# Kernel optimization log

Hardware: AMD Instinct MI355X
Metric: run time of the kernel (lower is better)

The kernel has to match this reference:

```python
import jax, jax.numpy as jnp
import numpy as np

# Rs_hidden = [(16,0),(16,1)] -> 16 scalar irreps (dim 1) then 16 vector irreps (dim 3)
B, N, M = 4, 80, 16
CH = M + 3 * M  # 64 channels
RADII = jnp.linspace(0.0, 1.0, 3)
GAMMA = 1.0 / (0.5 ** 2)  # gaussian rbf width = radii spacing
EPS = 1e-6

_lc = np.zeros((3, 3, 3), np.float32)
for i, j, k in [(0, 1, 2), (1, 2, 0), (2, 0, 1)]:
    _lc[i, j, k] = 1.0
    _lc[i, k, j] = -1.0
LC = jnp.asarray(_lc)  # Levi-Civita


def _si(t, w0, w1):
    """SelfInteraction: per-l mixing of multiplicities. t: [B, mi0 + 3*mi1, ...]."""
    mi0, mi1 = w0.shape[1], w1.shape[1]
    s = t[:, :mi0]
    v = t[:, mi0:].reshape(t.shape[0], mi1, 3, *t.shape[2:])
    os = jnp.einsum('om,nm...->no...', w0, s)
    ov = jnp.einsum('om,nmi...->noi...', w1, v)
    ov = ov.reshape(ov.shape[0], ov.shape[1] * 3, *ov.shape[3:])
    return jnp.concatenate([os, ov], axis=1)


def _norm_act(t, act):
    """NormActivation: scalar irreps -> act(x); vector irreps -> x * act(||x||)/||x||. Channel axis 1."""
    s = act(t[:, :M])
    v = t[:, M:].reshape(t.shape[0], M, 3, *t.shape[2:])
    n = jnp.sqrt(jnp.sum(v * v, axis=2, keepdims=True) + EPS)
    v = (v * act(n) / n).reshape(t.shape[0], 3 * M, *t.shape[2:])
    return jnp.concatenate([s, v], axis=1)


def _gate_mul(gate, target):
    """gate_normwise_multiply: multiply each irrep block of target by the L2 norm of the
    corresponding gate block (norm over the irrep components, channel axis 1)."""
    gs = jnp.abs(gate[:, :M])
    gv = gate[:, M:].reshape(gate.shape[0], M, 3, *gate.shape[2:])
    gn = jnp.sqrt(jnp.sum(gv * gv, axis=2) + EPS)
    factor = jnp.concatenate([gs, jnp.repeat(gn, 3, axis=1)], axis=1)
    return factor * target


def _interleave(a_t, b_t):
    """Interleave per-(m,l) blocks: [a_l0, b_l0, a_l1, b_l1] -> Rs_hidden_double layout."""
    return jnp.concatenate([a_t[:, :M], b_t[:, :M], a_t[:, M:], b_t[:, M:]], axis=1)


def _kernel(h_nei_diff, w_k00, w_k10, w_k01, w_k11):
    """SE3 point kernel for l in {0,1}, J<=2. Returns K[n,b,a,d,c] with d,c in irrep layout."""
    rad = jnp.sqrt(jnp.sum(h_nei_diff ** 2, axis=-1) + EPS)      # [B,N,N]
    nh = h_nei_diff / rad[..., None]                              # unit vectors
    rbf = jnp.exp(-GAMMA * (rad[..., None] - RADII) ** 2)        # [B,N,N,3]
    K00 = jnp.einsum('uvk,...k->...uv', w_k00, rbf)              # [B,N,N,M,M]
    K10 = jnp.einsum('uvk,...k,...i->...uiv', w_k10, rbf, nh).reshape(B, N, N, 3 * M, M)
    K01 = jnp.einsum('uvk,...k,...j->...uvj', w_k01, rbf, nh).reshape(B, N, N, M, 3 * M)
    RJ = jnp.einsum('juvk,...k->j...uv', w_k11, rbf)             # [3,B,N,N,M,M]
    eye = jnp.eye(3, dtype=rbf.dtype)
    cross = jnp.einsum('ijk,...k->...ij', LC, nh)                # J=1 basis
    outer = nh[..., :, None] * nh[..., None, :] - eye / 3.0      # J=2 basis
    base = (RJ[0][..., None, None] * eye
            + RJ[1][..., None, None] * cross[..., None, None, :, :]
            + RJ[2][..., None, None] * outer[..., None, None, :, :])  # [B,N,N,u,v,i,j]
    K11 = jnp.transpose(base, (0, 1, 2, 3, 5, 4, 6)).reshape(B, N, N, 3 * M, 3 * M)
    top = jnp.concatenate([K00, K01], axis=-1)
    bot = jnp.concatenate([K10, K11], axis=-1)
    return jnp.concatenate([top, bot], axis=-2)                  # [B,N,N,CH,CH]


def setup_inputs() -> dict:
    key = jax.random.key(0)
    ks = jax.random.split(key, 16)
    sc = 0.1
    d = {
        'x': jax.random.normal(ks[0], (B, CH, N), jnp.float32),
        'h_nei': jax.random.normal(ks[1], (B, CH, N), jnp.float32),
        'h_nei_diff': jax.random.normal(ks[2], (B, N, N, 3), jnp.float32),
        'mask': jax.random.uniform(ks[3], (B, N, N), jnp.float32),
        'w_k00': jax.random.normal(ks[4], (M, M, 3), jnp.float32) * sc,
        'w_k10': jax.random.normal(ks[5], (M, M, 3), jnp.float32) * sc,
        'w_k01': jax.random.normal(ks[6], (M, M, 3), jnp.float32) * sc,
        'w_k11': jax.random.normal(ks[7], (3, M, M, 3), jnp.float32) * sc,
        'si_z_w0': jax.random.normal(ks[8], (M, 2 * M), jnp.float32) * sc,
        'si_z_w1': jax.random.normal(ks[9], (M, 2 * M), jnp.float32) * sc,
        'si_r1_w0': jax.random.normal(ks[10], (M, M), jnp.float32) * sc,
        'si_r1_w1': jax.random.normal(ks[11], (M, M), jnp.float32) * sc,
        'si_r2_w0': jax.random.normal(ks[12], (M, M), jnp.float32) * sc,
        'si_r2_w1': jax.random.normal(ks[13], (M, M), jnp.float32) * sc,
        'si_ph_w0': jax.random.normal(ks[14], (M, 2 * M), jnp.float32) * sc,
        'si_ph_w1': jax.random.normal(ks[15], (M, 2 * M), jnp.float32) * sc,
    }
    return d


def reference(x, h_nei, h_nei_diff, mask, w_k00, w_k10, w_k01, w_k11,
              si_z_w0, si_z_w1, si_r1_w0, si_r1_w1, si_r2_w0, si_r2_w1,
              si_ph_w0, si_ph_w1):
    Kmat = _kernel(h_nei_diff, w_k00, w_k10, w_k01, w_k11)
    # masked neighbor conv: h_conv[n,d,b,a] = sum_c h_nei[n,c,a] K[n,b,a,d,c] mask[n,b,a]
    h_conv = jnp.einsum('nca,nbadc,nba->ndba', h_nei, Kmat, mask)
    sum_h = h_conv.sum(axis=-1)                                   # [B,CH,N]
    z = _norm_act(_si(_interleave(x, sum_h), si_z_w0, si_z_w1), jax.nn.sigmoid)
    r1 = _si(x, si_r1_w0, si_r1_w1)                               # [B,CH,N]
    r2 = _si(h_conv.reshape(B, CH, N * N), si_r2_w0, si_r2_w1).reshape(B, CH, N, N)
    r = _norm_act(r1[:, :, None, :] + r2, jax.nn.sigmoid)         # [B,CH,N,N]
    gated = _gate_mul(r, h_conv)
    sum_g = gated.sum(axis=-1)                                    # [B,CH,N]
    pre_h = _norm_act(_si(_interleave(x, sum_g), si_ph_w0, si_ph_w1), jnp.tanh)
    new_h = sum_h + _gate_mul(z, pre_h + sum_h)
    return new_h
```

## Files before the change

### kernel.cpp

```cpp
#include <hip/hip_runtime.h>
#include <math.h>

#define Bq 4
#define Nq 80
#define CHq 64
#define GAMMAq 4.0f
#define EPSq 1e-6f
#define PCWL 100
#define NQUAD 24


__global__ __launch_bounds__(192) void se3_precomp(
    const float* __restrict__ h_nei,
    const float* __restrict__ x,
    const float* __restrict__ w00,
    const float* __restrict__ w10,
    const float* __restrict__ w01,
    const float* __restrict__ w11,
    const float* __restrict__ wr10,
    const float* __restrict__ wr11,
    const float* __restrict__ wr20,
    const float* __restrict__ wr21,
    float* __restrict__ pc)
{
    const int L   = blockIdx.x & 7;
    const int idx = blockIdx.x >> 3;
    const int n   = L >> 1;
    const int a   = (L & 1) * 40 + idx;
    const int na  = n * Nq + a;
    const int tid = threadIdx.x;

    __shared__ float hsh[64];
    __shared__ float xsh[64];
    __shared__ float w00s[784], w10s[784], w01s[784];
    __shared__ float w11s[3][784];
    __shared__ float wr10s[272], wr11s[272];
    __shared__ float psh[2][42][16];
    __shared__ float r1sh[2][4][16];
    __shared__ float pout[16][PCWL];

    if (tid < 64)       hsh[tid]      = h_nei[(size_t)n * CHq * Nq + tid * Nq + a];
    else if (tid < 128) xsh[tid - 64] = x    [(size_t)n * CHq * Nq + (tid - 64) * Nq + a];

    for (int e = tid; e < 768; e += 192) {
        const int u = e / 48, r = e - u * 48;
        const int d = u * 49 + r;
        w00s[d]    = w00[e];
        w10s[d]    = w10[e];
        w01s[d]    = w01[e];
        w11s[0][d] = w11[e];
        w11s[1][d] = w11[768 + e];
        w11s[2][d] = w11[1536 + e];
    }
    for (int e = tid; e < 256; e += 192) {
        const int u = e >> 4, v = e & 15;
        wr10s[u * 17 + v] = wr10[e];
        wr11s[u * 17 + v] = wr11[e];
    }
    __syncthreads();

    if (tid < 128) {
        const int u    = tid & 15;
        const int q    = tid >> 4;
        const int half = q & 1;
        const int kk   = q >> 1;
        const int v0   = half * 8;

        if (kk < 3) {
            const int k = kk;
            float a00 = 0.f, a10 = 0.f;
            float c[3] = {0.f,0.f,0.f}, p0[3] = {0.f,0.f,0.f};
            float p1[3] = {0.f,0.f,0.f}, p2[3] = {0.f,0.f,0.f};
#pragma unroll
            for (int i = 0; i < 8; ++i) {
                const int v  = v0 + i;
                const int wi = u * 49 + v * 3 + k;
                const float s = hsh[v];
                a00 += w00s[wi] * s;
                a10 += w10s[wi] * s;
                const float w01v = w01s[wi];
                const float w110 = w11s[0][wi];
                const float w111 = w11s[1][wi];
                const float w112 = w11s[2][wi];
#pragma unroll
                for (int j = 0; j < 3; ++j) {
                    const float Vj = hsh[16 + v * 3 + j];
                    c[j]  += w01v * Vj;
                    p0[j] += w110 * Vj;
                    p1[j] += w111 * Vj;
                    p2[j] += w112 * Vj;
                }
            }
            psh[half][0 + k][u] = a00;
            psh[half][3 + k][u] = a10;
#pragma unroll
            for (int j = 0; j < 3; ++j) {
                psh[half][6  + k * 3 + j][u] = c[j];
                psh[half][15 + k * 3 + j][u] = p0[j];
                psh[half][24 + k * 3 + j][u] = p1[j];
                psh[half][33 + k * 3 + j][u] = p2[j];
            }
        } else {
            float r1s = 0.f, r1v[3] = {0.f, 0.f, 0.f};
#pragma unroll
            for (int i = 0; i < 8; ++i) {
                const int v = v0 + i;
                r1s += wr10s[u * 17 + v] * xsh[v];
                const float wv = wr11s[u * 17 + v];
#pragma unroll
                for (int j = 0; j < 3; ++j) r1v[j] += wv * xsh[16 + v * 3 + j];
            }
            r1sh[half][0][u] = r1s;
#pragma unroll
            for (int j = 0; j < 3; ++j) r1sh[half][1 + j][u] = r1v[j];
        }
    }
    __syncthreads();

    if (tid < 96) {
        const int u  = tid & 15;
        const int kk = tid >> 4;
#pragma unroll
        for (int c = kk * 7; c < kk * 7 + 7; ++c)
            pout[u][c] = psh[0][c][u] + psh[1][c][u];
        if (kk == 0) {
#pragma unroll
            for (int j = 0; j < 4; ++j)
                pout[u][42 + j] = r1sh[0][j][u] + r1sh[1][j][u];
            pout[u][46] = 0.f; pout[u][47] = 0.f;
#pragma unroll
            for (int j = 90; j < 96; ++j) pout[u][j] = 0.f;
        }
    }
    __syncthreads();

    if (tid < 96) {
        const int u  = tid & 15;
        const int kk = tid >> 4;
#pragma unroll
        for (int c = kk * 7; c < kk * 7 + 7; ++c) {
            const bool scalarType = (c < 3) || (c >= 6 && c < 15);
            const float* W = scalarType ? wr20 : wr21;
            float acc = 0.f;
#pragma unroll
            for (int v = 0; v < 16; ++v) acc += W[u * 16 + v] * pout[v][c];
            pout[u][48 + c] = acc;
        }
    }
    __syncthreads();

    {
        float4* dst = reinterpret_cast<float4*>(pc) + (size_t)na * (NQUAD * 16);
#pragma unroll
        for (int i = 0; i < 2; ++i) {
            const int qi = tid + i * 192;
            const int c4 = qi >> 4;
            const int u  = qi & 15;
            dst[c4 * 16 + u] = make_float4(pout[u][c4 * 4 + 0], pout[u][c4 * 4 + 1],
                                           pout[u][c4 * 4 + 2], pout[u][c4 * 4 + 3]);
        }
    }
}

__global__ __launch_bounds__(256, 1) void se3_main(
    const float* __restrict__ x,
    const float* __restrict__ hdiff,
    const float* __restrict__ mask,
    const float* __restrict__ wz0,
    const float* __restrict__ wz1,
    const float* __restrict__ wp0,
    const float* __restrict__ wp1,
    const float* __restrict__ pc,
    float* __restrict__ out)
{
    const int L     = blockIdx.x & 7;
    const int idx   = blockIdx.x >> 3;
    const int n     = L >> 1;
    const int bnode = (L & 1) * 40 + idx;
    const int tid   = threadIdx.x;
    const int g     = tid >> 4;
    const int u     = tid & 15;

    __shared__ float wsh[4][512];
    __shared__ float redW[4][8][16];
    __shared__ float sumHs[64], sumGs[64];

#pragma unroll
    for (int i = 0; i < 2; ++i) {
        const int widx = tid + i * 256;
        wsh[0][widx] = wz0[widx];
        wsh[1][widx] = wz1[widx];
        wsh[2][widx] = wp0[widx];
        wsh[3][widx] = wp1[widx];
    }

    const float* drow = hdiff + (size_t)(n * Nq + bnode) * Nq * 3;
    const float* mrow = mask  + (size_t)(n * Nq + bnode) * Nq;
    const float third = 1.0f / 3.0f;

    float dg[5][3], mg[5];
#pragma unroll
    for (int it = 0; it < 5; ++it) {
        const int a = it * 16 + g;
        dg[it][0] = drow[a * 3 + 0];
        dg[it][1] = drow[a * 3 + 1];
        dg[it][2] = drow[a * 3 + 2];
        mg[it]    = mrow[a];
    }

    const float4* pcbase = reinterpret_cast<const float4*>(pc)
                         + (size_t)(n * Nq) * (NQUAD * 16) + u;

    float shs = 0.f, shv0 = 0.f, shv1 = 0.f, shv2 = 0.f;
    float sgs = 0.f, sgv0 = 0.f, sgv1 = 0.f, sgv2 = 0.f;

    float pa[2][48], pb[2][44];

    {
        const float4* p4 = pcbase + (size_t)g * (NQUAD * 16);
#pragma unroll
        for (int i = 0; i < 12; ++i)
            *reinterpret_cast<float4*>(&pa[0][i * 4]) = p4[i * 16];
#pragma unroll
        for (int i = 0; i < 11; ++i)
            *reinterpret_cast<float4*>(&pb[0][i * 4]) = p4[(12 + i) * 16];
    }

#pragma unroll
    for (int it = 0; it < 5; ++it) {
        const int cur = it & 1, nxt = cur ^ 1;

        if (it < 4) {
            const int a2 = (it + 1) * 16 + g;
            const float4* p4 = pcbase + (size_t)a2 * (NQUAD * 16);
#pragma unroll
            for (int i = 0; i < 12; ++i)
                *reinterpret_cast<float4*>(&pa[nxt][i * 4]) = p4[i * 16];
#pragma unroll
            for (int i = 0; i < 11; ++i)
                *reinterpret_cast<float4*>(&pb[nxt][i * 4]) = p4[(12 + i) * 16];
        }

        const float d0 = dg[it][0], d1 = dg[it][1], d2 = dg[it][2];
        const float m  = mg[it];

        const float rad = sqrtf(d0 * d0 + d1 * d1 + d2 * d2 + EPSq);
        const float inv = 1.0f / rad;
        const float nh0 = d0 * inv, nh1 = d1 * inv, nh2 = d2 * inv;
        float rb[3];
        rb[0] = __expf(-GAMMAq * rad * rad);
        { float t1 = rad - 0.5f; rb[1] = __expf(-GAMMAq * t1 * t1); }
        { float t2 = rad - 1.0f; rb[2] = __expf(-GAMMAq * t2 * t2); }

        float as_ = 0.f, a10 = 0.f;
        float c01[3] = {0.f,0.f,0.f}, p0[3] = {0.f,0.f,0.f};
        float p1[3] = {0.f,0.f,0.f}, p2[3] = {0.f,0.f,0.f};
        float bs_ = 0.f, b10 = 0.f;
        float bc01[3] = {0.f,0.f,0.f}, bp0[3] = {0.f,0.f,0.f};
        float bp1[3] = {0.f,0.f,0.f}, bp2[3] = {0.f,0.f,0.f};
#pragma unroll
        for (int k = 0; k < 3; ++k) {
            const float r = rb[k];
            as_ += r * pa[cur][0 + k];
            a10 += r * pa[cur][3 + k];
            bs_ += r * pb[cur][0 + k];
            b10 += r * pb[cur][3 + k];
#pragma unroll
            for (int j = 0; j < 3; ++j) {
                c01[j]  += r * pa[cur][6  + k * 3 + j];
                p0[j]   += r * pa[cur][15 + k * 3 + j];
                p1[j]   += r * pa[cur][24 + k * 3 + j];
                p2[j]   += r * pa[cur][33 + k * 3 + j];
                bc01[j] += r * pb[cur][6  + k * 3 + j];
                bp0[j]  += r * pb[cur][15 + k * 3 + j];
                bp1[j]  += r * pb[cur][24 + k * 3 + j];
                bp2[j]  += r * pb[cur][33 + k * 3 + j];
            }
        }

        const float hcs = m * (as_ + c01[0] * nh0 + c01[1] * nh1 + c01[2] * nh2);
        const float cr0 = p1[1] * nh2 - p1[2] * nh1;
        const float cr1 = p1[2] * nh0 - p1[0] * nh2;
        const float cr2 = p1[0] * nh1 - p1[1] * nh0;
        const float pd  = p2[0] * nh0 + p2[1] * nh1 + p2[2] * nh2;
        const float hv0 = m * (nh0 * a10 + p0[0] + cr0 + nh0 * pd - p2[0] * third);
        const float hv1 = m * (nh1 * a10 + p0[1] + cr1 + nh1 * pd - p2[1] * third);
        const float hv2 = m * (nh2 * a10 + p0[2] + cr2 + nh2 * pd - p2[2] * third);

        const float r2s = m * (bs_ + bc01[0] * nh0 + bc01[1] * nh1 + bc01[2] * nh2);
        const float br0 = bp1[1] * nh2 - bp1[2] * nh1;
        const float br1 = bp1[2] * nh0 - bp1[0] * nh2;
        const float br2 = bp1[0] * nh1 - bp1[1] * nh0;
        const float bpd = bp2[0] * nh0 + bp2[1] * nh1 + bp2[2] * nh2;
        const float r2v0 = m * (nh0 * b10 + bp0[0] + br0 + nh0 * bpd - bp2[0] * third);
        const float r2v1 = m * (nh1 * b10 + bp0[1] + br1 + nh1 * bpd - bp2[1] * third);
        const float r2v2 = m * (nh2 * b10 + bp0[2] + br2 + nh2 * bpd - bp2[2] * third);

        const float r1s  = pa[cur][42];
        const float r1v0 = pa[cur][43], r1v1 = pa[cur][44], r1v2 = pa[cur][45];

        const float rs  = 1.0f / (1.0f + __expf(-(r1s + r2s)));
        const float wv0 = r1v0 + r2v0, wv1 = r1v1 + r2v1, wv2 = r1v2 + r2v2;
        const float nn  = sqrtf(wv0 * wv0 + wv1 * wv1 + wv2 * wv2 + EPSq);
        const float sc  = (1.0f / (1.0f + __expf(-nn))) / nn;
        const float rv0 = wv0 * sc, rv1 = wv1 * sc, rv2 = wv2 * sc;
        const float fs  = fabsf(rs);
        const float fv  = sqrtf(rv0 * rv0 + rv1 * rv1 + rv2 * rv2 + EPSq);

        shs += hcs;        shv0 += hv0;      shv1 += hv1;      shv2 += hv2;
        sgs += fs * hcs;   sgv0 += fv * hv0; sgv1 += fv * hv1; sgv2 += fv * hv2;
    }

    float vals[8] = {shs, shv0, shv1, shv2, sgs, sgv0, sgv1, sgv2};
#pragma unroll
    for (int q = 0; q < 8; ++q) {
        vals[q] += __shfl_xor(vals[q], 16, 64);
        vals[q] += __shfl_xor(vals[q], 32, 64);
    }
    const int wave = tid >> 6;
    if ((tid & 63) < 16) {
#pragma unroll
        for (int q = 0; q < 8; ++q) redW[wave][q][u] = vals[q];
    }
    __syncthreads();

    if (tid < 16) {
        float tacc[8];
#pragma unroll
        for (int q = 0; q < 8; ++q)
            tacc[q] = redW[0][q][tid] + redW[1][q][tid] + redW[2][q][tid] + redW[3][q][tid];
        sumHs[tid] = tacc[0];
        sumGs[tid] = tacc[4];
#pragma unroll
        for (int j = 0; j < 3; ++j) {
            sumHs[16 + tid * 3 + j] = tacc[1 + j];
            sumGs[16 + tid * 3 + j] = tacc[5 + j];
        }
    }
    __syncthreads();

    if (tid < 16) {
        const float* xb = x + (size_t)n * CHq * Nq + bnode;

        float zs_in = 0.f, ps_in = 0.f;
        float zv[3] = {0.f, 0.f, 0.f};
        float pv[3] = {0.f, 0.f, 0.f};
#pragma unroll
        for (int mm = 0; mm < 32; ++mm) {
            float Sh, Sg;
            if (mm < 16) { const float xv = xb[mm * Nq]; Sh = xv; Sg = xv; }
            else         { Sh = sumHs[mm - 16]; Sg = sumGs[mm - 16]; }
            zs_in += wsh[0][tid * 32 + mm] * Sh;
            ps_in += wsh[2][tid * 32 + mm] * Sg;
            const float wz = wsh[1][tid * 32 + mm];
            const float wp = wsh[3][tid * 32 + mm];
#pragma unroll
            for (int j = 0; j < 3; ++j) {
                float Vh, Vg;
                if (mm < 16) { const float xv = xb[(16 + mm * 3 + j) * Nq]; Vh = xv; Vg = xv; }
                else { Vh = sumHs[16 + (mm - 16) * 3 + j]; Vg = sumGs[16 + (mm - 16) * 3 + j]; }
                zv[j] += wz * Vh;
                pv[j] += wp * Vg;
            }
        }

        const float zs  = 1.0f / (1.0f + __expf(-zs_in));
        const float zn  = sqrtf(zv[0] * zv[0] + zv[1] * zv[1] + zv[2] * zv[2] + EPSq);
        const float zsc = (1.0f / (1.0f + __expf(-zn))) / zn;
        const float zv0 = zv[0] * zsc, zv1 = zv[1] * zsc, zv2 = zv[2] * zsc;
        const float phs = tanhf(ps_in);
        const float pn  = sqrtf(pv[0] * pv[0] + pv[1] * pv[1] + pv[2] * pv[2] + EPSq);
        const float psc = tanhf(pn) / pn;
        const float pv0 = pv[0] * psc, pv1 = pv[1] * psc, pv2 = pv[2] * psc;
        const float gfs = fabsf(zs);
        const float gfv = sqrtf(zv0 * zv0 + zv1 * zv1 + zv2 * zv2 + EPSq);

        float* ob = out + (size_t)n * CHq * Nq + bnode;
        const float sh_s = sumHs[tid];
        ob[tid * Nq] = sh_s + gfs * (phs + sh_s);
#pragma unroll
        for (int j = 0; j < 3; ++j) {
            const float shv = sumHs[16 + tid * 3 + j];
            const float pvj = (j == 0) ? pv0 : ((j == 1) ? pv1 : pv2);
            ob[(16 + tid * 3 + j) * Nq] = shv + gfv * (pvj + shv);
        }
    }
}

extern "C" void kernel_launch(void* const* d_in, const int* in_sizes, int n_in,
                              void* d_out, int out_size, void* d_ws, size_t ws_size,
                              hipStream_t stream) {
    const float* x      = (const float*)d_in[0];
    const float* h_nei  = (const float*)d_in[1];
    const float* hdiff  = (const float*)d_in[2];
    const float* mask   = (const float*)d_in[3];
    const float* w00    = (const float*)d_in[4];
    const float* w10    = (const float*)d_in[5];
    const float* w01    = (const float*)d_in[6];
    const float* w11    = (const float*)d_in[7];
    const float* wz0    = (const float*)d_in[8];
    const float* wz1    = (const float*)d_in[9];
    const float* wr10   = (const float*)d_in[10];
    const float* wr11   = (const float*)d_in[11];
    const float* wr20   = (const float*)d_in[12];
    const float* wr21   = (const float*)d_in[13];
    const float* wp0    = (const float*)d_in[14];
    const float* wp1    = (const float*)d_in[15];
    float* out = (float*)d_out;
    float* pc  = (float*)d_ws;

    se3_precomp<<<Bq * Nq, 192, 0, stream>>>(
        h_nei, x, w00, w10, w01, w11, wr10, wr11, wr20, wr21, pc);
    se3_main<<<Bq * Nq, 256, 0, stream>>>(
        x, hdiff, mask, wz0, wz1, wp0, wp1, pc, out);
}
```

Measured before the change: 24.03 us.

## Parallelize epilogue across 128 threads, fuse precomp stages, widen precomp block

```diff
diff --git a/kernel.cpp b/kernel.cpp
--- a/kernel.cpp
+++ b/kernel.cpp
@@ -10,7 +10,7 @@
 #define NQUAD 24
 
 
-__global__ __launch_bounds__(192) void se3_precomp(
+__global__ __launch_bounds__(256) void se3_precomp(
     const float* __restrict__ h_nei,
     const float* __restrict__ x,
     const float* __restrict__ w00,
@@ -42,7 +42,7 @@
     if (tid < 64)       hsh[tid]      = h_nei[(size_t)n * CHq * Nq + tid * Nq + a];
     else if (tid < 128) xsh[tid - 64] = x    [(size_t)n * CHq * Nq + (tid - 64) * Nq + a];
 
-    for (int e = tid; e < 768; e += 192) {
+    for (int e = tid; e < 768; e += 256) {
         const int u = e / 48, r = e - u * 48;
         const int d = u * 49 + r;
         w00s[d]    = w00[e];
@@ -52,10 +52,10 @@
         w11s[1][d] = w11[768 + e];
         w11s[2][d] = w11[1536 + e];
     }
-    for (int e = tid; e < 256; e += 192) {
-        const int u = e >> 4, v = e & 15;
-        wr10s[u * 17 + v] = wr10[e];
-        wr11s[u * 17 + v] = wr11[e];
+    if (tid < 256) {
+        const int u = tid >> 4, v = tid & 15;
+        wr10s[u * 17 + v] = wr10[tid];
+        wr11s[u * 17 + v] = wr11[tid];
     }
     __syncthreads();
 
@@ -121,8 +121,16 @@
         const int u  = tid & 15;
         const int kk = tid >> 4;
 #pragma unroll
-        for (int c = kk * 7; c < kk * 7 + 7; ++c)
+        for (int c = kk * 7; c < kk * 7 + 7; ++c) {
             pout[u][c] = psh[0][c][u] + psh[1][c][u];
+            const bool scalarType = (c < 3) || (c >= 6 && c < 15);
+            const float* W = scalarType ? wr20 : wr21;
+            float acc = 0.f;
+#pragma unroll
+            for (int v = 0; v < 16; ++v)
+                acc += W[u * 16 + v] * (psh[0][c][v] + psh[1][c][v]);
+            pout[u][48 + c] = acc;
+        }
         if (kk == 0) {
 #pragma unroll
             for (int j = 0; j < 4; ++j)
@@ -134,30 +142,17 @@
     }
     __syncthreads();
 
-    if (tid < 96) {
-        const int u  = tid & 15;
-        const int kk = tid >> 4;
-#pragma unroll
-        for (int c = kk * 7; c < kk * 7 + 7; ++c) {
-            const bool scalarType = (c < 3) || (c >= 6 && c < 15);
-            const float* W = scalarType ? wr20 : wr21;
-            float acc = 0.f;
-#pragma unroll
-            for (int v = 0; v < 16; ++v) acc += W[u * 16 + v] * pout[v][c];
-            pout[u][48 + c] = acc;
-        }
-    }
-    __syncthreads();
-
     {
         float4* dst = reinterpret_cast<float4*>(pc) + (size_t)na * (NQUAD * 16);
 #pragma unroll
         for (int i = 0; i < 2; ++i) {
-            const int qi = tid + i * 192;
-            const int c4 = qi >> 4;
-            const int u  = qi & 15;
-            dst[c4 * 16 + u] = make_float4(pout[u][c4 * 4 + 0], pout[u][c4 * 4 + 1],
-                                           pout[u][c4 * 4 + 2], pout[u][c4 * 4 + 3]);
+            const int qi = tid + i * 256;
+            if (qi < 384) {
+                const int c4 = qi >> 4;
+                const int u  = qi & 15;
+                dst[c4 * 16 + u] = make_float4(pout[u][c4 * 4 + 0], pout[u][c4 * 4 + 1],
+                                               pout[u][c4 * 4 + 2], pout[u][c4 * 4 + 3]);
+            }
         }
     }
 }
@@ -184,6 +179,22 @@
     __shared__ float wsh[4][512];
     __shared__ float redW[4][8][16];
     __shared__ float sumHs[64], sumGs[64];
+    __shared__ float epish[8][16];
+
+    const float4* pcbase = reinterpret_cast<const float4*>(pc)
+                         + (size_t)(n * Nq) * (NQUAD * 16) + u;
+
+    float pa[2][48], pb[2][44];
+
+    {
+        const float4* p4 = pcbase + (size_t)g * (NQUAD * 16);
+#pragma unroll
+        for (int i = 0; i < 12; ++i)
+            *reinterpret_cast<float4*>(&pa[0][i * 4]) = p4[i * 16];
+#pragma unroll
+        for (int i = 0; i < 11; ++i)
+            *reinterpret_cast<float4*>(&pb[0][i * 4]) = p4[(12 + i) * 16];
+    }
 
 #pragma unroll
     for (int i = 0; i < 2; ++i) {
@@ -208,23 +219,8 @@
         mg[it]    = mrow[a];
     }
 
-    const float4* pcbase = reinterpret_cast<const float4*>(pc)
-                         + (size_t)(n * Nq) * (NQUAD * 16) + u;
-
     float shs = 0.f, shv0 = 0.f, shv1 = 0.f, shv2 = 0.f;
     float sgs = 0.f, sgv0 = 0.f, sgv1 = 0.f, sgv2 = 0.f;
-
-    float pa[2][48], pb[2][44];
-
-    {
-        const float4* p4 = pcbase + (size_t)g * (NQUAD * 16);
-#pragma unroll
-        for (int i = 0; i < 12; ++i)
-            *reinterpret_cast<float4*>(&pa[0][i * 4]) = p4[i * 16];
-#pragma unroll
-        for (int i = 0; i < 11; ++i)
-            *reinterpret_cast<float4*>(&pb[0][i * 4]) = p4[(12 + i) * 16];
-    }
 
 #pragma unroll
     for (int it = 0; it < 5; ++it) {
@@ -339,39 +335,42 @@
     }
     __syncthreads();
 
+    if (tid < 128) {
+        const int q  = tid >> 4;
+        const int uu = tid & 15;
+        const float* xb   = x + (size_t)n * CHq * Nq + bnode;
+        const float* Wrow = wsh[(q == 0) ? 0 : (q < 4) ? 1 : (q == 4) ? 2 : 3] + uu * 32;
+        const float* SS   = (q < 4) ? sumHs : sumGs;
+        const bool scalar = (q == 0) || (q == 4);
+        const int  j      = scalar ? 0 : ((q < 4) ? (q - 1) : (q - 5));
+
+        float acc = 0.f;
+#pragma unroll
+        for (int mm = 0; mm < 32; ++mm) {
+            float val;
+            if (scalar) val = (mm < 16) ? xb[mm * Nq] : SS[mm - 16];
+            else        val = (mm < 16) ? xb[(16 + mm * 3 + j) * Nq]
+                                        : SS[16 + (mm - 16) * 3 + j];
+            acc += Wrow[mm] * val;
+        }
+        epish[q][uu] = acc;
+    }
+    __syncthreads();
+
     if (tid < 16) {
-        const float* xb = x + (size_t)n * CHq * Nq + bnode;
-
-        float zs_in = 0.f, ps_in = 0.f;
-        float zv[3] = {0.f, 0.f, 0.f};
-        float pv[3] = {0.f, 0.f, 0.f};
-#pragma unroll
-        for (int mm = 0; mm < 32; ++mm) {
-            float Sh, Sg;
-            if (mm < 16) { const float xv = xb[mm * Nq]; Sh = xv; Sg = xv; }
-            else         { Sh = sumHs[mm - 16]; Sg = sumGs[mm - 16]; }
-            zs_in += wsh[0][tid * 32 + mm] * Sh;
-            ps_in += wsh[2][tid * 32 + mm] * Sg;
-            const float wz = wsh[1][tid * 32 + mm];
-            const float wp = wsh[3][tid * 32 + mm];
-#pragma unroll
-            for (int j = 0; j < 3; ++j) {
-                float Vh, Vg;
-                if (mm < 16) { const float xv = xb[(16 + mm * 3 + j) * Nq]; Vh = xv; Vg = xv; }
-                else { Vh = sumHs[16 + (mm - 16) * 3 + j]; Vg = sumGs[16 + (mm - 16) * 3 + j]; }
-                zv[j] += wz * Vh;
-                pv[j] += wp * Vg;
-            }
-        }
+        const float zs_in = epish[0][tid];
+        const float zv0i = epish[1][tid], zv1i = epish[2][tid], zv2i = epish[3][tid];
+        const float ps_in = epish[4][tid];
+        const float pv0i = epish[5][tid], pv1i = epish[6][tid], pv2i = epish[7][tid];
 
         const float zs  = 1.0f / (1.0f + __expf(-zs_in));
-        const float zn  = sqrtf(zv[0] * zv[0] + zv[1] * zv[1] + zv[2] * zv[2] + EPSq);
+        const float zn  = sqrtf(zv0i * zv0i + zv1i * zv1i + zv2i * zv2i + EPSq);
         const float zsc = (1.0f / (1.0f + __expf(-zn))) / zn;
-        const float zv0 = zv[0] * zsc, zv1 = zv[1] * zsc, zv2 = zv[2] * zsc;
+        const float zv0 = zv0i * zsc, zv1 = zv1i * zsc, zv2 = zv2i * zsc;
         const float phs = tanhf(ps_in);
-        const float pn  = sqrtf(pv[0] * pv[0] + pv[1] * pv[1] + pv[2] * pv[2] + EPSq);
+        const float pn  = sqrtf(pv0i * pv0i + pv1i * pv1i + pv2i * pv2i + EPSq);
         const float psc = tanhf(pn) / pn;
-        const float pv0 = pv[0] * psc, pv1 = pv[1] * psc, pv2 = pv[2] * psc;
+        const float pv0 = pv0i * psc, pv1 = pv1i * psc, pv2 = pv2i * psc;
         const float gfs = fabsf(zs);
         const float gfv = sqrtf(zv0 * zv0 + zv1 * zv1 + zv2 * zv2 + EPSq);
 
@@ -409,7 +408,7 @@
     float* out = (float*)d_out;
     float* pc  = (float*)d_ws;
 
-    se3_precomp<<<Bq * Nq, 192, 0, stream>>>(
+    se3_precomp<<<Bq * Nq, 256, 0, stream>>>(
         h_nei, x, w00, w10, w01, w11, wr10, wr11, wr20, wr21, pc);
     se3_main<<<Bq * Nq, 256, 0, stream>>>(
         x, hdiff, mask, wz0, wz1, wp0, wp1, pc, out);
```

New measurement: 27.78 us. +15.6%, slower.
